# Kernel optimization log

Hardware: AMD Instinct MI355X
Metric: run time of the kernel (lower is better)

## Reference

```python
import jax, jax.numpy as jnp
import numpy as np

D_MODEL = 1024
NUM_HEADS = 16
D_H = D_MODEL // NUM_HEADS
BATCH, SEQ = 4, 2048


def setup_inputs() -> dict:
    key = jax.random.key(0)
    kx, kq, kk, kv, ko = jax.random.split(key, 5)
    sigma = (2.0 / (D_MODEL + D_MODEL)) ** 0.5

    def trunc(k):
        return jax.random.truncated_normal(k, -3.0, 3.0, (D_MODEL, D_MODEL), dtype=jnp.float32) * sigma

    return {
        "x": jax.random.normal(kx, (BATCH, SEQ, D_MODEL), dtype=jnp.float32),
        "Wq": trunc(kq),
        "Wk": trunc(kk),
        "Wv": trunc(kv),
        "Wo": trunc(ko),
    }


def reference(x, Wq, Wk, Wv, Wo):
    B, S, D = x.shape
    H, Dh = NUM_HEADS, D_H
    # Linear: einsum('d_out d_in, ... d_in -> ... d_out')
    q = jnp.einsum('oi,bsi->bso', Wq, x)
    k = jnp.einsum('oi,bsi->bso', Wk, x)
    v = jnp.einsum('oi,bsi->bso', Wv, x)
    # split heads: [B, H, S, Dh]
    q = q.reshape(B, S, H, Dh).transpose(0, 2, 1, 3)
    k = k.reshape(B, S, H, Dh).transpose(0, 2, 1, 3)
    v = v.reshape(B, S, H, Dh).transpose(0, 2, 1, 3)
    scale = 1.0 / jnp.sqrt(jnp.asarray(Dh, dtype=x.dtype))
    score = jnp.einsum('bhnd,bhmd->bhnm', q, k) * scale  # [B,H,S,S]
    causal = jnp.tril(jnp.ones((S, S), dtype=bool))
    score = jnp.where(causal, score, -jnp.inf)
    attn = jax.nn.softmax(score, axis=-1)
    out = jnp.einsum('bhnm,bhmd->bhnd', attn, v)
    out = out.transpose(0, 2, 1, 3).reshape(B, S, D)
    return jnp.einsum('oi,bsi->bso', Wo, out)
```

## Files before the change

kernel.cpp:

```cpp
#include <hip/hip_runtime.h>
#include <hip/hip_bf16.h>

typedef __bf16 bf16x8 __attribute__((ext_vector_type(8)));
typedef __bf16 bf16x4 __attribute__((ext_vector_type(4)));
typedef float f32x4 __attribute__((ext_vector_type(4)));
typedef float f32x16 __attribute__((ext_vector_type(16)));

#define NB 4
#define NS 2048
#define ND 1024
#define NH 16
#define NDH 64
#define NM (NB*NS)

#define MFMA(a,b,c)   __builtin_amdgcn_mfma_f32_16x16x32_bf16((a),(b),(c),0,0,0)
#define MFMA32(a,b,c) __builtin_amdgcn_mfma_f32_32x32x16_bf16((a),(b),(c),0,0,0)

__device__ __forceinline__ void gload16(const void* g, void* l) {
    __builtin_amdgcn_global_load_lds(
        (const __attribute__((address_space(1))) void*)(g),
        (__attribute__((address_space(3))) void*)(l),
        16, 0, 0);
}

__device__ __forceinline__ unsigned cvt_pk_bf16(float lo, float hi) {
    unsigned w;
    asm("v_cvt_pk_bf16_f32 %0, %1, %2" : "=v"(w) : "v"(lo), "v"(hi));
    return w;
}
__device__ __forceinline__ float fmax3(float a, float b, float c) {
    float d;
    asm("v_max3_f32 %0, %1, %2, %3" : "=v"(d) : "v"(a), "v"(b), "v"(c));
    return d;
}
#define PLSWAP(a, b) asm("v_permlane32_swap_b32 %0, %1" : "+v"(a), "+v"(b))

__global__ __launch_bounds__(256) void cast4(const float* __restrict__ in,
                                             __bf16* __restrict__ out, int n) {
    int i = (blockIdx.x * 256 + threadIdx.x) * 4;
    if (i >= n) return;
    float4 v = *(const float4*)(in + i);
    bf16x4 o;
    o[0] = (__bf16)v.x; o[1] = (__bf16)v.y; o[2] = (__bf16)v.z; o[3] = (__bf16)v.w;
    *(bf16x4*)(out + i) = o;
}

__global__ __launch_bounds__(256) void cast4w(
    const float* __restrict__ w0, const float* __restrict__ w1,
    const float* __restrict__ w2, const float* __restrict__ w3,
    __bf16* __restrict__ o0, __bf16* __restrict__ o1,
    __bf16* __restrict__ o2, __bf16* __restrict__ o3) {
    const int z = blockIdx.y;
    const float* in  = (z == 0) ? w0 : (z == 1) ? w1 : (z == 2) ? w2 : w3;
    __bf16*      out = (z == 0) ? o0 : (z == 1) ? o1 : (z == 2) ? o2 : o3;
    int i = (blockIdx.x * 256 + threadIdx.x) * 4;
    float4 v = *(const float4*)(in + i);
    bf16x4 o;
    o[0] = (__bf16)v.x; o[1] = (__bf16)v.y; o[2] = (__bf16)v.z; o[3] = (__bf16)v.w;
    *(bf16x4*)(out + i) = o;
}

template<int MODE>
__global__ __launch_bounds__(256) void gemm128(
    const __bf16* __restrict__ A,
    const __bf16* __restrict__ W0, const __bf16* __restrict__ W1,
    const __bf16* __restrict__ W2,
    __bf16* __restrict__ O0, __bf16* __restrict__ O1, __bf16* __restrict__ O2,
    float* __restrict__ Cf)
{
    __shared__ alignas(16) __bf16 SB[2 * 128 * 32];
    __bf16* As = SB;
    __bf16* Bs = SB + 128 * 32;

    const int tid  = threadIdx.x;
    const int wave = tid >> 6, lane = tid & 63;
    const int l16  = lane & 15, lq = lane >> 4;
    const int bm = blockIdx.x * 128;
    const int bn = blockIdx.y * 128;
    const int z  = (MODE == 0) ? blockIdx.z : 0;
    const __bf16* __restrict__ Bw =
        (MODE == 0) ? ((z == 0) ? W0 : (z == 1) ? W1 : W2) : W0;

    const int wr = (wave >> 1) * 64;
    const int wc = (wave & 1) * 64;

    f32x4 acc[4][4];
    #pragma unroll
    for (int i = 0; i < 4; i++)
        #pragma unroll
        for (int j = 0; j < 4; j++)
            acc[i][j] = (f32x4){0.f, 0.f, 0.f, 0.f};

    const int ch0 = tid, ch1 = tid + 256;
    const int r0 = ch0 >> 2, c0 = (ch0 & 3) * 8;
    const int r1 = ch1 >> 2, c1 = (ch1 & 3) * 8;

    for (int k0 = 0; k0 < ND; k0 += 32) {
        __syncthreads();
        gload16(A  + (size_t)(bm + r0) * ND + k0 + c0, As + ch0 * 8);
        gload16(Bw + (size_t)(bn + r0) * ND + k0 + c0, Bs + ch0 * 8);
        gload16(A  + (size_t)(bm + r1) * ND + k0 + c1, As + ch1 * 8);
        gload16(Bw + (size_t)(bn + r1) * ND + k0 + c1, Bs + ch1 * 8);
        __syncthreads();

        bf16x8 af[4], bf[4];
        #pragma unroll
        for (int i = 0; i < 4; i++) {
            af[i] = *(const bf16x8*)(As + (wr + i*16 + l16) * 32 + lq * 8);
            bf[i] = *(const bf16x8*)(Bs + (wc + i*16 + l16) * 32 + lq * 8);
        }
        #pragma unroll
        for (int i = 0; i < 4; i++)
            #pragma unroll
            for (int j = 0; j < 4; j++)
                acc[i][j] = MFMA(af[i], bf[j], acc[i][j]);
    }

    if (MODE == 0 && z == 2) {
        __bf16* T = SB;
        const int TP = 136;
        #pragma unroll 1
        for (int c = 0; c < 4; ++c) {
            __syncthreads();
            #pragma unroll
            for (int j = 0; j < 4; j++) {
                if (((wc + j * 16) >> 5) != c) continue;
                #pragma unroll
                for (int i = 0; i < 4; i++)
                    #pragma unroll
                    for (int r = 0; r < 4; r++) {
                        int row = wr + i*16 + lq*4 + r;
                        int col = wc + j*16 + l16 - c*32;
                        T[col * TP + row] = (__bf16)acc[i][j][r];
                    }
            }
            __syncthreads();
            #pragma unroll
            for (int u2 = 0; u2 < 2; u2++) {
                int idx  = tid + u2 * 256;
                int trow = idx >> 4, tu = idx & 15;
                int gcol = bn + c*32 + trow;
                int gs   = bm + tu * 8;
                bf16x8 val = *(const bf16x8*)&T[trow * TP + tu * 8];
                int hh = gcol >> 6, dh = gcol & 63;
                *(bf16x8*)&O2[(((size_t)(gs >> 11) * NH + hh) * NDH + dh) * NS
                              + (gs & 2047)] = val;
            }
        }
        return;
    }

    #pragma unroll
    for (int i = 0; i < 4; i++) {
        #pragma unroll
        for (int j = 0; j < 4; j++) {
            #pragma unroll
            for (int r = 0; r < 4; r++) {
                int row = bm + wr + i*16 + lq*4 + r;
                int col = bn + wc + j*16 + l16;
                float v = acc[i][j][r];
                if (MODE == 1) {
                    Cf[(size_t)row * ND + col] = v;
                } else {
                    if (z == 0) v *= 0.1803368801111204f;
                    int b = row >> 11, s = row & 2047;
                    int h = col >> 6,  dh = col & 63;
                    __bf16* dst = (z == 0) ? O0 : O1;
                    dst[(((size_t)b*NH + h)*NS + s)*NDH + dh] = (__bf16)v;
                }
            }
        }
    }
}

__global__ __launch_bounds__(256) void attn_st(
    const __bf16* __restrict__ Q, const __bf16* __restrict__ K,
    const __bf16* __restrict__ Vt, __bf16* __restrict__ Oa)
{
    __shared__ alignas(16) __bf16 Ks[32*64];
    __shared__ alignas(16) __bf16 Vs[64*32];
    __shared__ float Fs[4][32];

    const int tid  = threadIdx.x;
    const int wave = tid >> 6, lane = tid & 63;
    const int qq   = lane & 31, hi = lane >> 5;

    const int bid = blockIdx.x;
    const int jg  = 15 - (bid >> 6);
    const int bh  = (bid & 7) * 8 + ((bid >> 3) & 7);
    const int j   = 4 * jg + wave;
    const int q0  = 32 * j;
    const int nt  = 4 * jg + 4;

    const int b = bh >> 4, h = bh & 15;
    const size_t qkb = (size_t)bh * NS * NDH;
    const size_t vbb = (size_t)bh * NDH * NS;
    float* Fw = Fs[wave];

    bf16x8 qf[4];
    {
        const __bf16* qr = Q + qkb + (size_t)(q0 + qq) * NDH + hi * 8;
        #pragma unroll
        for (int c = 0; c < 4; c++) qf[c] = *(const bf16x8*)(qr + c * 16);
    }

    f32x16 o0 = (f32x16)0.f, o1 = (f32x16)0.f;
    float mr = -__builtin_inff(), lsum = 0.f;

    const int kr = tid >> 3, ku = tid & 7;
    const int vd = tid >> 2, vu = tid & 3;
    const __bf16* ksrc = K  + qkb + (size_t)kr * NDH + (size_t)((ku ^ (kr & 7)) * 8);
    const __bf16* vsrc = Vt + vbb + (size_t)vd * NS  + (size_t)((vu ^ ((vd >> 1) & 3)) * 8);
    __bf16* kdst = Ks + tid * 8;
    __bf16* vdst = Vs + tid * 8;

    const int vsw = (qq >> 1) & 3;

    #pragma unroll 1
    for (int t = 0; t < nt; ++t) {
        __syncthreads();
        gload16(ksrc, kdst);
        gload16(vsrc, vdst);
        asm volatile("s_waitcnt vmcnt(0)" ::: "memory");
        __syncthreads();

        if (t <= j) {
            bf16x8 kf[4], vf[4];
            #pragma unroll
            for (int c = 0; c < 4; c++)
                kf[c] = *(const bf16x8*)(Ks + qq * 64 + ((2 * c + hi) ^ (qq & 7)) * 8);
            vf[0] = *(const bf16x8*)(Vs + qq * 32        + ((hi)     ^ vsw) * 8);
            vf[1] = *(const bf16x8*)(Vs + qq * 32        + ((2 + hi) ^ vsw) * 8);
            vf[2] = *(const bf16x8*)(Vs + (qq + 32) * 32 + ((hi)     ^ vsw) * 8);
            vf[3] = *(const bf16x8*)(Vs + (qq + 32) * 32 + ((2 + hi) ^ vsw) * 8);

            f32x16 s = (f32x16)0.f;
            __builtin_amdgcn_s_setprio(1);
            #pragma unroll
            for (int c = 0; c < 4; c++) s = MFMA32(kf[c], qf[c], s);
            __builtin_amdgcn_s_setprio(0);

            if (t == j) {
                #pragma unroll
                for (int r = 0; r < 16; r++) {
                    const int crow = (r & 3) + 8 * (r >> 2) + 4 * hi;
                    if (crow > qq) s[r] = -__builtin_inff();
                }
            }

            float a0 = fmax3(s[0],  s[1],  s[2]);
            float a1 = fmax3(s[3],  s[4],  s[5]);
            float a2 = fmax3(s[6],  s[7],  s[8]);
            float a3 = fmax3(s[9],  s[10], s[11]);
            float a4 = fmax3(s[12], s[13], s[14]);
            float tm = fmaxf(fmax3(a0, a1, a2), fmax3(a3, a4, s[15]));

            if (__any(tm > mr + 8.f)) {
                float rowm = fmaxf(tm, __shfl_xor(tm, 32));
                float mnew = fmaxf(mr, rowm);
                float fac  = exp2f(mr - mnew);
                mr = mnew; lsum *= fac;
                if (lane < 32) Fw[qq] = fac;
                f32x4 f0 = *(const f32x4*)&Fw[4 * hi];
                f32x4 f1 = *(const f32x4*)&Fw[8 + 4 * hi];
                f32x4 f2 = *(const f32x4*)&Fw[16 + 4 * hi];
                f32x4 f3 = *(const f32x4*)&Fw[24 + 4 * hi];
                #pragma unroll
                for (int i = 0; i < 4; i++) {
                    o0[i]      *= f0[i]; o1[i]      *= f0[i];
                    o0[4 + i]  *= f1[i]; o1[4 + i]  *= f1[i];
                    o0[8 + i]  *= f2[i]; o1[8 + i]  *= f2[i];
                    o0[12 + i] *= f3[i]; o1[12 + i] *= f3[i];
                }
            }

            float pv[16]; float psum = 0.f;
            #pragma unroll
            for (int r = 0; r < 16; r++) { pv[r] = exp2f(s[r] - mr); psum += pv[r]; }
            lsum += psum;

            unsigned w0 = cvt_pk_bf16(pv[0],  pv[1]);
            unsigned w1 = cvt_pk_bf16(pv[2],  pv[3]);
            unsigned w2 = cvt_pk_bf16(pv[4],  pv[5]);
            unsigned w3 = cvt_pk_bf16(pv[6],  pv[7]);
            unsigned w4 = cvt_pk_bf16(pv[8],  pv[9]);
            unsigned w5 = cvt_pk_bf16(pv[10], pv[11]);
            unsigned w6 = cvt_pk_bf16(pv[12], pv[13]);
            unsigned w7 = cvt_pk_bf16(pv[14], pv[15]);
            PLSWAP(w0, w2); PLSWAP(w1, w3);
            PLSWAP(w4, w6); PLSWAP(w5, w7);
            bf16x8 pa0 = __builtin_bit_cast(bf16x8, (uint4){w0, w1, w2, w3});
            bf16x8 pa1 = __builtin_bit_cast(bf16x8, (uint4){w4, w5, w6, w7});

            __builtin_amdgcn_s_setprio(1);
            o0 = MFMA32(pa0, vf[0], o0);
            o0 = MFMA32(pa1, vf[1], o0);
            o1 = MFMA32(pa0, vf[2], o1);
            o1 = MFMA32(pa1, vf[3], o1);
            __builtin_amdgcn_s_setprio(0);
        }

        ksrc += 32 * NDH;
        vsrc += 32;
    }

    lsum += __shfl_xor(lsum, 32);
    if (lane < 32) Fw[qq] = 1.f / lsum;
    f32x4 i0 = *(const f32x4*)&Fw[4 * hi];
    f32x4 i1 = *(const f32x4*)&Fw[8 + 4 * hi];
    f32x4 i2 = *(const f32x4*)&Fw[16 + 4 * hi];
    f32x4 i3 = *(const f32x4*)&Fw[24 + 4 * hi];
    __bf16* ob = Oa + ((size_t)b * NS + q0) * ND + h * 64 + qq;
    #pragma unroll
    for (int g2 = 0; g2 < 4; g2++) {
        f32x4 iv = (g2 == 0) ? i0 : (g2 == 1) ? i1 : (g2 == 2) ? i2 : i3;
        #pragma unroll
        for (int i = 0; i < 4; i++) {
            const int row = 8 * g2 + 4 * hi + i;
            ob[(size_t)row * ND]      = (__bf16)(o0[4 * g2 + i] * iv[i]);
            ob[(size_t)row * ND + 32] = (__bf16)(o1[4 * g2 + i] * iv[i]);
        }
    }
}

extern "C" void kernel_launch(void* const* d_in, const int* in_sizes, int n_in,
                              void* d_out, int out_size, void* d_ws, size_t ws_size,
                              hipStream_t stream) {
    const float* x  = (const float*)d_in[0];
    const float* wq = (const float*)d_in[1];
    const float* wk = (const float*)d_in[2];
    const float* wv = (const float*)d_in[3];
    const float* wo = (const float*)d_in[4];
    char* ws = (char*)d_ws;

    __bf16* xb  = (__bf16*)(ws);
    __bf16* wqb = (__bf16*)(ws + (16ull << 20));
    __bf16* wkb = (__bf16*)(ws + (18ull << 20));
    __bf16* wvb = (__bf16*)(ws + (20ull << 20));
    __bf16* wob = (__bf16*)(ws + (22ull << 20));
    __bf16* Qb  = (__bf16*)(ws + (24ull << 20));
    __bf16* Kb  = (__bf16*)(ws + (40ull << 20));
    __bf16* Vtb = (__bf16*)(ws + (56ull << 20));
    __bf16* Ab  = (__bf16*)(ws + (72ull << 20));
    float* out  = (float*)d_out;

    cast4<<<dim3(NM * ND / 1024), 256, 0, stream>>>(x, xb, NM * ND);
    cast4w<<<dim3(ND * ND / 1024, 4), 256, 0, stream>>>(
        wq, wk, wv, wo, wqb, wkb, wvb, wob);

    gemm128<0><<<dim3(NM/128, ND/128, 3), 256, 0, stream>>>(
        xb, wqb, wkb, wvb, Qb, Kb, Vtb, nullptr);

    attn_st<<<dim3(1024), 256, 0, stream>>>(Qb, Kb, Vtb, Ab);

    gemm128<1><<<dim3(NM/128, ND/128), 256, 0, stream>>>(
        Ab, wob, nullptr, nullptr, nullptr, nullptr, nullptr, out);
}
```

Baseline: 186.9 us.

## Replace projection GEMMs with double-buffered 256x128 swizzled LDS pipeline

Rewrites the QKV and output projection GEMM as a 512-thread kernel with 256x128 output tiles and a K-step of 64. LDS is double-buffered, and the next tile's global-to-LDS loads are interleaved between MFMA phases. LDS rows use an XOR swizzle to avoid bank conflicts, and s_setprio raises wave priority during MFMA bursts. The aim is to hide global load latency and cut the per-iteration barrier overhead of the old single-buffer 128x128 loop. In exchange it uses 96KB of LDS, which lowers occupancy, and halves the number of blocks.

```diff
diff --git a/kernel.cpp b/kernel.cpp
--- a/kernel.cpp
+++ b/kernel.cpp
@@ -61,21 +61,22 @@
 }
 
 template<int MODE>
-__global__ __launch_bounds__(256) void gemm128(
+__global__ __launch_bounds__(512) void gemmfp(
     const __bf16* __restrict__ A,
     const __bf16* __restrict__ W0, const __bf16* __restrict__ W1,
     const __bf16* __restrict__ W2,
     __bf16* __restrict__ O0, __bf16* __restrict__ O1, __bf16* __restrict__ O2,
     float* __restrict__ Cf)
 {
-    __shared__ alignas(16) __bf16 SB[2 * 128 * 32];
-    __bf16* As = SB;
-    __bf16* Bs = SB + 128 * 32;
+    __shared__ alignas(16) __bf16 As0[256*64];
+    __shared__ alignas(16) __bf16 As1[256*64];
+    __shared__ alignas(16) __bf16 Bs0[128*64];
+    __shared__ alignas(16) __bf16 Bs1[128*64];
 
     const int tid  = threadIdx.x;
     const int wave = tid >> 6, lane = tid & 63;
     const int l16  = lane & 15, lq = lane >> 4;
-    const int bm = blockIdx.x * 128;
+    const int bm = blockIdx.x * 256;
     const int bn = blockIdx.y * 128;
     const int z  = (MODE == 0) ? blockIdx.z : 0;
     const __bf16* __restrict__ Bw =
@@ -91,34 +92,87 @@
         for (int j = 0; j < 4; j++)
             acc[i][j] = (f32x4){0.f, 0.f, 0.f, 0.f};
 
-    const int ch0 = tid, ch1 = tid + 256;
-    const int r0 = ch0 >> 2, c0 = (ch0 & 3) * 8;
-    const int r1 = ch1 >> 2, c1 = (ch1 & 3) * 8;
-
-    for (int k0 = 0; k0 < ND; k0 += 32) {
-        __syncthreads();
-        gload16(A  + (size_t)(bm + r0) * ND + k0 + c0, As + ch0 * 8);
-        gload16(Bw + (size_t)(bn + r0) * ND + k0 + c0, Bs + ch0 * 8);
-        gload16(A  + (size_t)(bm + r1) * ND + k0 + c1, As + ch1 * 8);
-        gload16(Bw + (size_t)(bn + r1) * ND + k0 + c1, Bs + ch1 * 8);
-        __syncthreads();
-
-        bf16x8 af[4], bf[4];
-        #pragma unroll
-        for (int i = 0; i < 4; i++) {
-            af[i] = *(const bf16x8*)(As + (wr + i*16 + l16) * 32 + lq * 8);
-            bf[i] = *(const bf16x8*)(Bs + (wc + i*16 + l16) * 32 + lq * 8);
-        }
-        #pragma unroll
-        for (int i = 0; i < 4; i++)
-            #pragma unroll
-            for (int j = 0; j < 4; j++)
-                acc[i][j] = MFMA(af[i], bf[j], acc[i][j]);
-    }
+    const int srow = tid >> 3;
+    const int au   = (tid & 7) ^ (srow & 7);
+    const __bf16* Ag = A  + (size_t)(bm + srow) * ND + au * 8;
+    const __bf16* Bg = Bw + (size_t)(bn + srow) * ND + au * 8;
+    size_t koff = 0;
+
+#define STA(DST, C) gload16(Ag + (size_t)(64*(C)) * ND + koff, (DST) + (tid + 512*(C)) * 8)
+#define STB(DST, C) gload16(Bg + (size_t)(64*(C)) * ND + koff, (DST) + (tid + 512*(C)) * 8)
+
+    const int asw = l16 & 7;
+
+#define GTILE(XA, XB, YA, YB, DOSTAGE)                                        \
+    {                                                                         \
+        bf16x8 af[4][2], bfr[2][2];                                           \
+                                                       \
+        _Pragma("unroll")                                                     \
+        for (int i = 0; i < 4; i++)                                           \
+            _Pragma("unroll")                                                 \
+            for (int kk = 0; kk < 2; kk++)                                    \
+                af[i][kk] = *(const bf16x8*)((XA) + (wr + i*16 + l16) * 64    \
+                                              + ((kk*4 + lq) ^ asw) * 8);     \
+        _Pragma("unroll")                                                     \
+        for (int j = 0; j < 2; j++)                                           \
+            _Pragma("unroll")                                                 \
+            for (int kk = 0; kk < 2; kk++)                                    \
+                bfr[j][kk] = *(const bf16x8*)((XB) + (wc + j*16 + l16) * 64   \
+                                               + ((kk*4 + lq) ^ asw) * 8);    \
+        if (DOSTAGE) { STA(YA, 0); STA(YA, 1); STA(YA, 2); }                  \
+        __builtin_amdgcn_s_barrier();                                         \
+        asm volatile("s_waitcnt lgkmcnt(0)" ::: "memory");                    \
+        __builtin_amdgcn_s_setprio(1);                                        \
+        _Pragma("unroll")                                                     \
+        for (int i = 0; i < 4; i++)                                           \
+            _Pragma("unroll")                                                 \
+            for (int j = 0; j < 2; j++) {                                     \
+                acc[i][j] = MFMA(af[i][0], bfr[j][0], acc[i][j]);             \
+                acc[i][j] = MFMA(af[i][1], bfr[j][1], acc[i][j]);             \
+            }                                                                 \
+        __builtin_amdgcn_s_setprio(0);                                        \
+        __builtin_amdgcn_s_barrier();                                         \
+                                      \
+        _Pragma("unroll")                                                     \
+        for (int j = 0; j < 2; j++)                                           \
+            _Pragma("unroll")                                                 \
+            for (int kk = 0; kk < 2; kk++)                                    \
+                bfr[j][kk] = *(const bf16x8*)((XB) + (wc + (j+2)*16 + l16) * 64 \
+                                               + ((kk*4 + lq) ^ asw) * 8);    \
+        if (DOSTAGE) { STA(YA, 3); STB(YB, 0); STB(YB, 1); koff += 64; }      \
+        __builtin_amdgcn_s_barrier();                                         \
+        asm volatile("s_waitcnt lgkmcnt(0)" ::: "memory");                    \
+        __builtin_amdgcn_s_setprio(1);                                        \
+        _Pragma("unroll")                                                     \
+        for (int i = 0; i < 4; i++)                                           \
+            _Pragma("unroll")                                                 \
+            for (int j = 0; j < 2; j++) {                                     \
+                acc[i][j+2] = MFMA(af[i][0], bfr[j][0], acc[i][j+2]);         \
+                acc[i][j+2] = MFMA(af[i][1], bfr[j][1], acc[i][j+2]);         \
+            }                                                                 \
+        __builtin_amdgcn_s_setprio(0);                                        \
+        asm volatile("s_waitcnt vmcnt(0)" ::: "memory");                      \
+        __builtin_amdgcn_s_barrier();                                         \
+    }
+
+    STA(As0, 0); STA(As0, 1); STA(As0, 2); STA(As0, 3);
+    STB(Bs0, 0); STB(Bs0, 1);
+    koff = 64;
+    asm volatile("s_waitcnt vmcnt(0)" ::: "memory");
+    __builtin_amdgcn_s_barrier();
+
+    #pragma unroll 1
+    for (int it = 0; it < 8; ++it) {
+        GTILE(As0, Bs0, As1, Bs1, 1)
+        GTILE(As1, Bs1, As0, Bs0, (it < 7))
+    }
+#undef GTILE
+#undef STA
+#undef STB
 
     if (MODE == 0 && z == 2) {
-        __bf16* T = SB;
-        const int TP = 136;
+        __bf16* T = As0;
+        const int TP = 264;
         #pragma unroll 1
         for (int c = 0; c < 4; ++c) {
             __syncthreads();
@@ -137,8 +191,8 @@
             __syncthreads();
             #pragma unroll
             for (int u2 = 0; u2 < 2; u2++) {
-                int idx  = tid + u2 * 256;
-                int trow = idx >> 4, tu = idx & 15;
+                int idx  = tid + u2 * 512;
+                int trow = idx >> 5, tu = idx & 31;
                 int gcol = bn + c*32 + trow;
                 int gs   = bm + tu * 8;
                 bf16x8 val = *(const bf16x8*)&T[trow * TP + tu * 8];
@@ -348,11 +402,11 @@
     cast4w<<<dim3(ND * ND / 1024, 4), 256, 0, stream>>>(
         wq, wk, wv, wo, wqb, wkb, wvb, wob);
 
-    gemm128<0><<<dim3(NM/128, ND/128, 3), 256, 0, stream>>>(
+    gemmfp<0><<<dim3(NM/256, ND/128, 3), 512, 0, stream>>>(
         xb, wqb, wkb, wvb, Qb, Kb, Vtb, nullptr);
 
     attn_st<<<dim3(1024), 256, 0, stream>>>(Qb, Kb, Vtb, Ab);
 
-    gemm128<1><<<dim3(NM/128, ND/128), 256, 0, stream>>>(
+    gemmfp<1><<<dim3(NM/256, ND/128), 512, 0, stream>>>(
         Ab, wob, nullptr, nullptr, nullptr, nullptr, nullptr, out);
 }
```

Result: slower. 194.8 us (+4.2%).
